# Kernel optimization log

Measured on AMD Instinct MI355X. Metric: run time of the kernel, lower is better.

The kernel has to match this reference:

```python
import jax, jax.numpy as jnp
import numpy as np

SCALE = 8.0  # sqrt(hid=64), passed as init arg `scale`


def setup_inputs() -> dict:
    key = jax.random.key(0)
    kq, kk, kv, km = jax.random.split(key, 4)
    B, S, H = 32, 2048, 64  # B = bs*n_head
    q = jax.random.normal(kq, (B, S, H), dtype=jnp.float32)
    k = jax.random.normal(kk, (B, S, H), dtype=jnp.float32)
    v = jax.random.normal(kv, (B, S, H), dtype=jnp.float32)
    mask = jax.random.bernoulli(km, 0.1, (B, S, S))  # True = masked out
    return {"q": q, "k": k, "v": v, "mask": mask, "cca": 0}


def reference(q, k, v, mask, cca):
    # scores: [B, Sq, Sk]
    attn = jnp.einsum('bqh,bkh->bqk', q, k) / SCALE
    if mask is not None:
        attn = jnp.where(mask, jnp.finfo(q.dtype).min, attn)
    if cca:
        # CCA branch: softmax over the query/sequence axis (dim=1)
        attn = jax.nn.softmax(attn, axis=1)
        ctx = jnp.einsum('bq,bkh->bqh', attn.squeeze(-1)[..., None].squeeze(-1), v) if attn.ndim == 2 else jnp.einsum('bqk,bkh->bqh', attn, v)
    else:
        attn = jax.nn.softmax(attn, axis=2)
        ctx = jnp.einsum('bqk,bkh->bqh', attn, v)  # [B, Sq, H]
    return (ctx, attn)
```

## Files before the change

### kernel.cpp

```cpp
#include <hip/hip_runtime.h>
#include <hip/hip_bf16.h>

typedef __bf16    bf16x8_t __attribute__((ext_vector_type(8)));
typedef float     f32x4_t  __attribute__((ext_vector_type(4)));
typedef short     s16x4_t  __attribute__((ext_vector_type(4)));
typedef short     s16x8_t  __attribute__((ext_vector_type(8)));
typedef unsigned  u32x4_t  __attribute__((ext_vector_type(4)));

#define S_LEN 2048
#define HDIM  64
#define BQ    32
#define NTHREADS 512
#define PSTR_B 4112
#define BMSTR 264

__device__ __forceinline__ short f2bf(float f) {
    return __builtin_bit_cast(short, (__bf16)f);
}
__device__ __forceinline__ float bf2f(short s) {
    return __builtin_bit_cast(float, ((unsigned)(unsigned short)s) << 16);
}
__device__ __forceinline__ short* pelem(short* P, int row, int e) {
    return (short*)((char*)P + (unsigned)row * PSTR_B + (unsigned)e * 2u);
}
__device__ __forceinline__ const short* pelemc(const short* P, int row, int e) {
    return pelem(const_cast<short*>(P), row, e);
}
__device__ __forceinline__ unsigned nzmask16(u32x4_t w) {
    unsigned n = 0;
    #pragma unroll
    for (int i = 0; i < 4; ++i) {
        const unsigned x = w[i];
        const unsigned t = (x & 0x7F7F7F7Fu) + 0x7F7F7F7Fu;
        const unsigned z = ((t | x) & 0x80808080u) >> 7;
        n |= ((z * 0x10204081u) >> 28) << (4 * i);
    }
    return n;
}
__device__ __forceinline__ unsigned nzmask4w(u32x4_t w) {
    return (w[0] ? 1u : 0u) | (w[1] ? 2u : 0u) | (w[2] ? 4u : 0u) | (w[3] ? 8u : 0u);
}

#define PK8(lo, hi, out8) { s16x8_t _t; \
    _t[0]=f2bf((lo)[0]); _t[1]=f2bf((lo)[1]); _t[2]=f2bf((lo)[2]); _t[3]=f2bf((lo)[3]); \
    _t[4]=f2bf((hi)[0]); _t[5]=f2bf((hi)[1]); _t[6]=f2bf((hi)[2]); _t[7]=f2bf((hi)[3]); \
    (out8) = __builtin_bit_cast(bf16x8_t, _t); }
#define PKV(src, dst) { s16x8_t _t; \
    _t[0]=f2bf((src)[0]); _t[1]=f2bf((src)[1]); _t[2]=f2bf((src)[2]); _t[3]=f2bf((src)[3]); \
    _t[4]=f2bf((src)[4]); _t[5]=f2bf((src)[5]); _t[6]=f2bf((src)[6]); _t[7]=f2bf((src)[7]); \
    (dst) = __builtin_bit_cast(bf16x8_t, _t); }

__global__ void detect_mask(const unsigned char* __restrict__ M, int* __restrict__ flags) {
    __shared__ int cnt[4];
    if (threadIdx.x < 4) cnt[threadIdx.x] = 0;
    __syncthreads();
    int local[4] = {0, 0, 0, 0};
    for (int i = threadIdx.x; i < 16384; i += 256)
        if (M[i]) local[i & 3]++;
    #pragma unroll
    for (int c = 0; c < 4; ++c)
        if (local[c]) atomicAdd(&cnt[c], local[c]);
    __syncthreads();
    if (threadIdx.x == 0) {
        int stride;
        if (cnt[1] == 0 && cnt[2] == 0 && cnt[3] == 0)      stride = 4;
        else if (cnt[0] == 0 && cnt[1] == 0)                stride = 4;
        else                                                stride = 1;
        flags[0] = stride;
    }
}

__global__ __launch_bounds__(NTHREADS, 2)
void sdpa_one(const float* __restrict__ Q, const float* __restrict__ K,
              const float* __restrict__ V, const unsigned char* __restrict__ M,
              const int* __restrict__ MF, float* __restrict__ OUT)
{
    __shared__ short Plds[BQ * (PSTR_B / 2)];
    __shared__ unsigned char Bm[BQ * BMSTR];
    __shared__ float Pvp[4][BQ][17];
    __shared__ float rowsum[BQ];
    __shared__ float rinv_s[BQ];

    const int tid  = threadIdx.x;
    const int w    = tid >> 6;
    const int lane = tid & 63;
    const int col  = lane & 15;
    const int kg   = lane >> 4;
    const int mstride = MF[0];

    const int id   = blockIdx.x;
    const int slot = id >> 3;
    const int b    = ((slot >> 6) << 3) | (id & 7);
    const int q0   = (slot & 63) * BQ;

    float* attn_out = OUT + (size_t)32 * S_LEN * HDIM;

    if (tid < BQ) rowsum[tid] = 0.f;

    {
        const int row  = tid >> 4;
        const int segE = (tid & 15) * 128;
        unsigned long long bits[2] = {0ull, 0ull};
        if (mstride == 1) {
            const unsigned char* mp = M + (size_t)b * S_LEN * S_LEN
                                        + (size_t)(q0 + row) * S_LEN + segE;
            #pragma unroll
            for (int j = 0; j < 8; ++j)
                bits[j >> 2] |= (unsigned long long)nzmask16(*(const u32x4_t*)(mp + j * 16))
                                << (16 * (j & 3));
        } else {
            const unsigned* mp = (const unsigned*)M + (size_t)b * S_LEN * S_LEN
                                   + (size_t)(q0 + row) * S_LEN + segE;
            #pragma unroll
            for (int j = 0; j < 32; ++j)
                bits[j >> 4] |= (unsigned long long)nzmask4w(*(const u32x4_t*)(mp + j * 4))
                                << (4 * (j & 15));
        }
        unsigned long long* bp = (unsigned long long*)&Bm[row * BMSTR + (tid & 15) * 16];
        bp[0] = bits[0]; bp[1] = bits[1];
    }

    bf16x8_t af[2][2];
    #pragma unroll
    for (int m = 0; m < 2; ++m)
        #pragma unroll
        for (int kk = 0; kk < 2; ++kk) {
            const float* qp = Q + ((size_t)b * S_LEN + q0 + m * 16 + col) * HDIM + kk * 32 + kg * 8;
            const f32x4_t qa = *(const f32x4_t*)qp;
            const f32x4_t qb = *(const f32x4_t*)(qp + 4);
            PK8(qa, qb, af[m][kk]);
        }
    __syncthreads();

    float rs[2][4] = {{0.f,0.f,0.f,0.f},{0.f,0.f,0.f,0.f}};
    {
        const float* Kb = K + (size_t)b * S_LEN * HDIM;
        f32x4_t A0,B0,C0,D0, A1,B1,C1,D1;
#define LDK(f, AX,BX,CX,DX) { \
    const float* kp = Kb + (size_t)(w * 256 + (f) * 16 + col) * HDIM + kg * 8; \
    AX = *(const f32x4_t*)kp;        BX = *(const f32x4_t*)(kp + 4); \
    CX = *(const f32x4_t*)(kp + 32); DX = *(const f32x4_t*)(kp + 36); }
#define STEP(f, AX,BX,CX,DX, PF, fp) { \
    bf16x8_t kb0, kb1; PK8(AX, BX, kb0); PK8(CX, DX, kb1); \
    if (PF) LDK(fp, AX,BX,CX,DX); \
    f32x4_t acc0 = {0.f,0.f,0.f,0.f}, acc1 = {0.f,0.f,0.f,0.f}; \
    acc0 = __builtin_amdgcn_mfma_f32_16x16x32_bf16(af[0][0], kb0, acc0, 0,0,0); \
    acc0 = __builtin_amdgcn_mfma_f32_16x16x32_bf16(af[0][1], kb1, acc0, 0,0,0); \
    acc1 = __builtin_amdgcn_mfma_f32_16x16x32_bf16(af[1][0], kb0, acc1, 0,0,0); \
    acc1 = __builtin_amdgcn_mfma_f32_16x16x32_bf16(af[1][1], kb1, acc1, 0,0,0); \
    const int c = w * 256 + (f) * 16 + col; \
    _Pragma("unroll") \
    for (int r = 0; r < 4; ++r) { \
        const int row0 = kg * 4 + r; \
        const unsigned b0m = Bm[row0 * BMSTR + (c >> 3)]; \
        const float p0 = ((b0m >> (c & 7)) & 1u) ? 0.f : __expf(acc0[r] * 0.125f); \
        rs[0][r] += p0; \
        *pelem(Plds, row0, c) = f2bf(p0); \
        const int row1 = 16 + kg * 4 + r; \
        const unsigned b1m = Bm[row1 * BMSTR + (c >> 3)]; \
        const float p1 = ((b1m >> (c & 7)) & 1u) ? 0.f : __expf(acc1[r] * 0.125f); \
        rs[1][r] += p1; \
        *pelem(Plds, row1, c) = f2bf(p1); \
    } }
        LDK(0, A0,B0,C0,D0);
        LDK(1, A1,B1,C1,D1);
        #pragma unroll
        for (int ff = 0; ff < 16; ff += 2) {
            STEP(ff,     A0,B0,C0,D0, (ff + 2 < 16), ff + 2);
            STEP(ff + 1, A1,B1,C1,D1, (ff + 3 < 16), ff + 3);
        }
#undef LDK
#undef STEP
    }
    #pragma unroll
    for (int m = 0; m < 2; ++m)
        #pragma unroll
        for (int r = 0; r < 4; ++r) {
            float s = rs[m][r];
            s += __shfl_xor(s, 1); s += __shfl_xor(s, 2);
            s += __shfl_xor(s, 4); s += __shfl_xor(s, 8);
            if (col == 0) atomicAdd(&rowsum[m * 16 + kg * 4 + r], s);
        }
    __syncthreads();
    if (tid < BQ) rinv_s[tid] = 1.0f / rowsum[tid];
    __syncthreads();

    const int hb    = (w & 3) * 16;
    const int kbase = (w >> 2) * 1024;
    const float* Vb = V + (size_t)b * S_LEN * HDIM;

    f32x4_t cacc0 = {0.f,0.f,0.f,0.f}, cacc1 = {0.f,0.f,0.f,0.f};
    {
        float vr0[8], vr1[8], vr2[8], vr3[8];
#define LOADV(kc, dst) { \
    const float* vp = Vb + (size_t)(kbase + (kc) * 32 + kg * 8) * HDIM + hb + col; \
    dst[0] = vp[0];        dst[1] = vp[HDIM];     dst[2] = vp[2*HDIM]; dst[3] = vp[3*HDIM]; \
    dst[4] = vp[4*HDIM];   dst[5] = vp[5*HDIM];   dst[6] = vp[6*HDIM]; dst[7] = vp[7*HDIM]; }
#define PVSTEP(kc, vsrc) { \
    bf16x8_t vbf; PKV(vsrc, vbf); \
    const int ke = kbase + (kc) * 32 + kg * 8; \
    const bf16x8_t pa0 = *(const bf16x8_t*)pelemc(Plds, col,      ke); \
    const bf16x8_t pa1 = *(const bf16x8_t*)pelemc(Plds, 16 + col, ke); \
    cacc0 = __builtin_amdgcn_mfma_f32_16x16x32_bf16(pa0, vbf, cacc0, 0,0,0); \
    cacc1 = __builtin_amdgcn_mfma_f32_16x16x32_bf16(pa1, vbf, cacc1, 0,0,0); }
        LOADV(0, vr0); LOADV(1, vr1); LOADV(2, vr2); LOADV(3, vr3);
        #pragma unroll
        for (int g = 0; g < 8; ++g) {
            PVSTEP(4 * g,     vr0); if (4 * g + 4 < 32) LOADV(4 * g + 4, vr0);
            PVSTEP(4 * g + 1, vr1); if (4 * g + 5 < 32) LOADV(4 * g + 5, vr1);
            PVSTEP(4 * g + 2, vr2); if (4 * g + 6 < 32) LOADV(4 * g + 6, vr2);
            PVSTEP(4 * g + 3, vr3); if (4 * g + 7 < 32) LOADV(4 * g + 7, vr3);
        }
#undef LOADV
#undef PVSTEP
    }

    {
        const int srow = w * 4 + kg;
        const float my_rinv = rinv_s[srow];
        float* abp = attn_out + ((size_t)b * S_LEN + q0 + srow) * S_LEN + col * 4;
        #pragma unroll 4
        for (int sec = 0; sec < 32; ++sec) {
            const s16x4_t pv = *(const s16x4_t*)pelemc(Plds, srow, sec * 64 + col * 4);
            f32x4_t o;
            o[0] = bf2f(pv[0]) * my_rinv; o[1] = bf2f(pv[1]) * my_rinv;
            o[2] = bf2f(pv[2]) * my_rinv; o[3] = bf2f(pv[3]) * my_rinv;
            *(f32x4_t*)(abp + sec * 64) = o;
        }
    }

    if (w >= 4) {
        #pragma unroll
        for (int r = 0; r < 4; ++r) {
            Pvp[w - 4][kg * 4 + r][col]      = cacc0[r];
            Pvp[w - 4][16 + kg * 4 + r][col] = cacc1[r];
        }
    }
    __syncthreads();
    if (w < 4) {
        #pragma unroll
        for (int r = 0; r < 4; ++r) {
            const int row0 = kg * 4 + r;
            const int row1 = 16 + kg * 4 + r;
            OUT[((size_t)b * S_LEN + q0 + row0) * HDIM + hb + col]
                = (cacc0[r] + Pvp[w][row0][col]) * rinv_s[row0];
            OUT[((size_t)b * S_LEN + q0 + row1) * HDIM + hb + col]
                = (cacc1[r] + Pvp[w][row1][col]) * rinv_s[row1];
        }
    }
}

extern "C" void kernel_launch(void* const* d_in, const int* in_sizes, int n_in,
                              void* d_out, int out_size, void* d_ws, size_t ws_size,
                              hipStream_t stream)
{
    const float* q = (const float*)d_in[0];
    const float* k = (const float*)d_in[1];
    const float* v = (const float*)d_in[2];
    const unsigned char* mask = (const unsigned char*)d_in[3];
    int* mflags = (int*)d_ws;
    float* out = (float*)d_out;
    detect_mask<<<dim3(1), dim3(256), 0, stream>>>(mask, mflags);
    sdpa_one<<<dim3(2048), dim3(NTHREADS), 0, stream>>>(q, k, v, mask, mflags, out);
}
```

Baseline: 444.9 us.

## Transpose QK MFMA output, vectorize P stores, deepen K and V prefetch

Swaps the MFMA operands so each lane holds four consecutive key columns of one query row. This lets the kernel read one mask word per row, write four bf16 probabilities to LDS in a single vector store, and cut the row-sum reduction to two cross-lane shuffles and two atomics per lane group. It also raises the K prefetch depth from 2 to 4 tiles and the V prefetch depth from 4 to 8 chunks, which raises register pressure and may reduce occupancy.

Result: faster. 431.4 us, median of 2 (-3.0%).

```diff
diff --git a/kernel.cpp b/kernel.cpp
--- a/kernel.cpp
+++ b/kernel.cpp
@@ -132,10 +132,10 @@
         }
     __syncthreads();
 
-    float rs[2][4] = {{0.f,0.f,0.f,0.f},{0.f,0.f,0.f,0.f}};
+    float rs0 = 0.f, rs1 = 0.f;
     {
         const float* Kb = K + (size_t)b * S_LEN * HDIM;
-        f32x4_t A0,B0,C0,D0, A1,B1,C1,D1;
+        f32x4_t A0,B0,C0,D0, A1,B1,C1,D1, A2,B2,C2,D2, A3,B3,C3,D3;
 #define LDK(f, AX,BX,CX,DX) { \
     const float* kp = Kb + (size_t)(w * 256 + (f) * 16 + col) * HDIM + kg * 8; \
     AX = *(const f32x4_t*)kp;        BX = *(const f32x4_t*)(kp + 4); \
@@ -144,43 +144,51 @@
     bf16x8_t kb0, kb1; PK8(AX, BX, kb0); PK8(CX, DX, kb1); \
     if (PF) LDK(fp, AX,BX,CX,DX); \
     f32x4_t acc0 = {0.f,0.f,0.f,0.f}, acc1 = {0.f,0.f,0.f,0.f}; \
-    acc0 = __builtin_amdgcn_mfma_f32_16x16x32_bf16(af[0][0], kb0, acc0, 0,0,0); \
-    acc0 = __builtin_amdgcn_mfma_f32_16x16x32_bf16(af[0][1], kb1, acc0, 0,0,0); \
-    acc1 = __builtin_amdgcn_mfma_f32_16x16x32_bf16(af[1][0], kb0, acc1, 0,0,0); \
-    acc1 = __builtin_amdgcn_mfma_f32_16x16x32_bf16(af[1][1], kb1, acc1, 0,0,0); \
-    const int c = w * 256 + (f) * 16 + col; \
-    _Pragma("unroll") \
-    for (int r = 0; r < 4; ++r) { \
-        const int row0 = kg * 4 + r; \
-        const unsigned b0m = Bm[row0 * BMSTR + (c >> 3)]; \
-        const float p0 = ((b0m >> (c & 7)) & 1u) ? 0.f : __expf(acc0[r] * 0.125f); \
-        rs[0][r] += p0; \
-        *pelem(Plds, row0, c) = f2bf(p0); \
-        const int row1 = 16 + kg * 4 + r; \
-        const unsigned b1m = Bm[row1 * BMSTR + (c >> 3)]; \
-        const float p1 = ((b1m >> (c & 7)) & 1u) ? 0.f : __expf(acc1[r] * 0.125f); \
-        rs[1][r] += p1; \
-        *pelem(Plds, row1, c) = f2bf(p1); \
-    } }
+    acc0 = __builtin_amdgcn_mfma_f32_16x16x32_bf16(kb0, af[0][0], acc0, 0,0,0); \
+    acc0 = __builtin_amdgcn_mfma_f32_16x16x32_bf16(kb1, af[0][1], acc0, 0,0,0); \
+    acc1 = __builtin_amdgcn_mfma_f32_16x16x32_bf16(kb0, af[1][0], acc1, 0,0,0); \
+    acc1 = __builtin_amdgcn_mfma_f32_16x16x32_bf16(kb1, af[1][1], acc1, 0,0,0); \
+    const int c0 = w * 256 + (f) * 16 + kg * 4; \
+    const int sh = c0 & 7;             \
+    { const unsigned bb = Bm[col * BMSTR + (c0 >> 3)]; \
+      float p0 = ((bb >> (sh    )) & 1u) ? 0.f : __expf(acc0[0] * 0.125f); \
+      float p1 = ((bb >> (sh + 1)) & 1u) ? 0.f : __expf(acc0[1] * 0.125f); \
+      float p2 = ((bb >> (sh + 2)) & 1u) ? 0.f : __expf(acc0[2] * 0.125f); \
+      float p3 = ((bb >> (sh + 3)) & 1u) ? 0.f : __expf(acc0[3] * 0.125f); \
+      rs0 += (p0 + p1) + (p2 + p3); \
+      s16x4_t pk; pk[0]=f2bf(p0); pk[1]=f2bf(p1); pk[2]=f2bf(p2); pk[3]=f2bf(p3); \
+      *(s16x4_t*)pelem(Plds, col, c0) = pk; } \
+    { const unsigned bb = Bm[(16 + col) * BMSTR + (c0 >> 3)]; \
+      float p0 = ((bb >> (sh    )) & 1u) ? 0.f : __expf(acc1[0] * 0.125f); \
+      float p1 = ((bb >> (sh + 1)) & 1u) ? 0.f : __expf(acc1[1] * 0.125f); \
+      float p2 = ((bb >> (sh + 2)) & 1u) ? 0.f : __expf(acc1[2] * 0.125f); \
+      float p3 = ((bb >> (sh + 3)) & 1u) ? 0.f : __expf(acc1[3] * 0.125f); \
+      rs1 += (p0 + p1) + (p2 + p3); \
+      s16x4_t pk; pk[0]=f2bf(p0); pk[1]=f2bf(p1); pk[2]=f2bf(p2); pk[3]=f2bf(p3); \
+      *(s16x4_t*)pelem(Plds, 16 + col, c0) = pk; } }
         LDK(0, A0,B0,C0,D0);
         LDK(1, A1,B1,C1,D1);
-        #pragma unroll
-        for (int ff = 0; ff < 16; ff += 2) {
-            STEP(ff,     A0,B0,C0,D0, (ff + 2 < 16), ff + 2);
-            STEP(ff + 1, A1,B1,C1,D1, (ff + 3 < 16), ff + 3);
+        LDK(2, A2,B2,C2,D2);
+        LDK(3, A3,B3,C3,D3);
+        #pragma unroll
+        for (int ff = 0; ff < 16; ff += 4) {
+            STEP(ff,     A0,B0,C0,D0, (ff + 4 < 16), ff + 4);
+            STEP(ff + 1, A1,B1,C1,D1, (ff + 5 < 16), ff + 5);
+            STEP(ff + 2, A2,B2,C2,D2, (ff + 6 < 16), ff + 6);
+            STEP(ff + 3, A3,B3,C3,D3, (ff + 7 < 16), ff + 7);
         }
 #undef LDK
 #undef STEP
     }
-    #pragma unroll
-    for (int m = 0; m < 2; ++m)
-        #pragma unroll
-        for (int r = 0; r < 4; ++r) {
-            float s = rs[m][r];
-            s += __shfl_xor(s, 1); s += __shfl_xor(s, 2);
-            s += __shfl_xor(s, 4); s += __shfl_xor(s, 8);
-            if (col == 0) atomicAdd(&rowsum[m * 16 + kg * 4 + r], s);
-        }
+    {
+        float s0 = rs0, s1 = rs1;
+        s0 += __shfl_xor(s0, 16); s0 += __shfl_xor(s0, 32);
+        s1 += __shfl_xor(s1, 16); s1 += __shfl_xor(s1, 32);
+        if (lane < 16) {
+            atomicAdd(&rowsum[col], s0);
+            atomicAdd(&rowsum[16 + col], s1);
+        }
+    }
     __syncthreads();
     if (tid < BQ) rinv_s[tid] = 1.0f / rowsum[tid];
     __syncthreads();
@@ -191,7 +199,7 @@
 
     f32x4_t cacc0 = {0.f,0.f,0.f,0.f}, cacc1 = {0.f,0.f,0.f,0.f};
     {
-        float vr0[8], vr1[8], vr2[8], vr3[8];
+        float vr0[8], vr1[8], vr2[8], vr3[8], vr4[8], vr5[8], vr6[8], vr7[8];
 #define LOADV(kc, dst) { \
     const float* vp = Vb + (size_t)(kbase + (kc) * 32 + kg * 8) * HDIM + hb + col; \
     dst[0] = vp[0];        dst[1] = vp[HDIM];     dst[2] = vp[2*HDIM]; dst[3] = vp[3*HDIM]; \
@@ -204,12 +212,17 @@
     cacc0 = __builtin_amdgcn_mfma_f32_16x16x32_bf16(pa0, vbf, cacc0, 0,0,0); \
     cacc1 = __builtin_amdgcn_mfma_f32_16x16x32_bf16(pa1, vbf, cacc1, 0,0,0); }
         LOADV(0, vr0); LOADV(1, vr1); LOADV(2, vr2); LOADV(3, vr3);
-        #pragma unroll
-        for (int g = 0; g < 8; ++g) {
-            PVSTEP(4 * g,     vr0); if (4 * g + 4 < 32) LOADV(4 * g + 4, vr0);
-            PVSTEP(4 * g + 1, vr1); if (4 * g + 5 < 32) LOADV(4 * g + 5, vr1);
-            PVSTEP(4 * g + 2, vr2); if (4 * g + 6 < 32) LOADV(4 * g + 6, vr2);
-            PVSTEP(4 * g + 3, vr3); if (4 * g + 7 < 32) LOADV(4 * g + 7, vr3);
+        LOADV(4, vr4); LOADV(5, vr5); LOADV(6, vr6); LOADV(7, vr7);
+        #pragma unroll
+        for (int gg = 0; gg < 4; ++gg) {
+            PVSTEP(8*gg,     vr0); if (8*gg +  8 < 32) LOADV(8*gg +  8, vr0);
+            PVSTEP(8*gg + 1, vr1); if (8*gg +  9 < 32) LOADV(8*gg +  9, vr1);
+            PVSTEP(8*gg + 2, vr2); if (8*gg + 10 < 32) LOADV(8*gg + 10, vr2);
+            PVSTEP(8*gg + 3, vr3); if (8*gg + 11 < 32) LOADV(8*gg + 11, vr3);
+            PVSTEP(8*gg + 4, vr4); if (8*gg + 12 < 32) LOADV(8*gg + 12, vr4);
+            PVSTEP(8*gg + 5, vr5); if (8*gg + 13 < 32) LOADV(8*gg + 13, vr5);
+            PVSTEP(8*gg + 6, vr6); if (8*gg + 14 < 32) LOADV(8*gg + 14, vr6);
+            PVSTEP(8*gg + 7, vr7); if (8*gg + 15 < 32) LOADV(8*gg + 15, vr7);
         }
 #undef LOADV
 #undef PVSTEP
```
